# Kernel optimization log

Measured on AMD Instinct MI355X. Metric: run time of the kernel, lower is better.

The kernel has to match this reference:

```python
import jax, jax.numpy as jnp
import numpy as np

POOL = 7  # adaptive_avg_pool2d output size (7,7)


def _bin_edges(start, length):
    """Adaptive-avg-pool bin boundaries.
    start, length: [N] int32 -> (lo, hi) each [N, POOL] absolute indices,
    matching torch: lo_i = floor(i*L/P), hi_i = ceil((i+1)*L/P).
    """
    i = jnp.arange(POOL, dtype=jnp.int32)
    lo = start[:, None] + (i[None, :] * length[:, None]) // POOL
    hi = start[:, None] + (-((-(i[None, :] + 1)) * length[:, None] // POOL))
    # note: ceil(a/b) = -(-a // b); written below explicitly
    hi = start[:, None] - ((-(i[None, :] + 1) * length[:, None]) // POOL)
    return lo, hi


def roi_adaptive_avg_pool(features, rois):
    """features: [1, C, H, W]; rois: [N, 4] int (x1,y1,x2,y2 inclusive).
    Returns [N, C, POOL, POOL] == torch stack of adaptive_avg_pool2d over
    features[:, :, y1:y2+1, x1:x2+1], vectorized via an integral image.
    """
    B, C, H, W = features.shape  # B == 1 (forced by shared_fcs input dim)
    # integral image with a zero row/col prepended: ii[y, x] = sum over [:y, :x]
    ii = jnp.cumsum(jnp.cumsum(features, axis=2), axis=3)
    ii = jnp.pad(ii, ((0, 0), (0, 0), (1, 0), (1, 0)))[0]  # [C, H+1, W+1]

    x1, y1, x2, y2 = rois[:, 0], rois[:, 1], rois[:, 2], rois[:, 3]
    ys, ye = _bin_edges(y1, y2 - y1 + 1)   # [N, POOL]
    xs, xe = _bin_edges(x1, x2 - x1 + 1)
    Y0, Y1 = ys[:, :, None], ye[:, :, None]   # [N, POOL, 1]
    X0, X1 = xs[:, None, :], xe[:, None, :]   # [N, 1, POOL]

    def gather(Y, X):
        return ii[:, Y, X]  # [C, N, POOL, POOL]

    sums = gather(Y1, X1) - gather(Y0, X1) - gather(Y1, X0) + gather(Y0, X0)
    area = ((Y1 - Y0) * (X1 - X0)).astype(features.dtype)  # [N, POOL, POOL]
    pooled = sums / area[None]                              # [C, N, POOL, POOL]
    return jnp.transpose(pooled, (1, 0, 2, 3))              # [N, C, POOL, POOL]


def setup_inputs() -> dict:
    key = jax.random.key(0)
    ks = jax.random.split(key, 12)
    C, H, W, N, F = 256, 336, 336, 2000, 256
    features = jax.random.normal(ks[0], (1, C, H, W), dtype=jnp.float32)
    # valid small ROIs (shuttlecock-sized), x1<=x2, y1<=y2, in-bounds
    x1 = jax.random.randint(ks[1], (N,), 0, W - 40)
    y1 = jax.random.randint(ks[2], (N,), 0, H - 40)
    bw = jax.random.randint(ks[3], (N,), 4, 40)
    bh = jax.random.randint(ks[4], (N,), 4, 40)
    rois = jnp.stack([x1, y1, jnp.minimum(x1 + bw, W - 1),
                      jnp.minimum(y1 + bh, H - 1)], axis=1).astype(jnp.int32)
    d_in = C * POOL * POOL
    w1 = jax.random.normal(ks[5], (d_in, F), dtype=jnp.float32) * (1.0 / np.sqrt(d_in))
    b1 = jnp.zeros((F,), dtype=jnp.float32)
    w2 = jax.random.normal(ks[6], (F, F), dtype=jnp.float32) * (1.0 / np.sqrt(F))
    b2 = jnp.zeros((F,), dtype=jnp.float32)
    w_cls = jax.random.normal(ks[7], (F, 2), dtype=jnp.float32) * 0.01
    b_cls = jnp.zeros((2,), dtype=jnp.float32)
    w_reg = jax.random.normal(ks[8], (F, 4), dtype=jnp.float32) * 0.001
    b_reg = jnp.zeros((4,), dtype=jnp.float32)
    return {"features": features, "rois": rois, "w1": w1, "b1": b1,
            "w2": w2, "b2": b2, "w_cls": w_cls, "b_cls": b_cls,
            "w_reg": w_reg, "b_reg": b_reg}


def reference(features, rois, w1, b1, w2, b2, w_cls, b_cls, w_reg, b_reg):
    roi_feats = roi_adaptive_avg_pool(features, rois)          # [N, C, 7, 7]
    roi_feats = roi_feats.reshape(roi_feats.shape[0], -1)      # [N, C*49]
    h = jax.nn.relu(roi_feats @ w1 + b1)
    h = jax.nn.relu(h @ w2 + b2)
    cls_score = h @ w_cls + b_cls                              # [N, num_classes+1]
    bbox_pred = h @ w_reg + b_reg                              # [N, 4]
    return (cls_score, bbox_pred)
```

## Files before the change

kernel.cpp:

```cpp
#include <hip/hip_runtime.h>

typedef unsigned int uint;
typedef unsigned short ushort;
typedef __bf16 v8bf __attribute__((ext_vector_type(8)));
typedef float v4f __attribute__((ext_vector_type(4)));

#define CCH 256
#define HH 336
#define WW 336
#define HWSZ (HH*WW)
#define NROI 2000
#define KDIM 12544
#define MPAD 2048
#define SPLITK 14
#define KSP (KDIM/SPLITK)

__device__ __forceinline__ ushort bf16r(float f) {
  uint u = __float_as_uint(f);
  u += 0x7fffu + ((u >> 16) & 1u);
  return (ushort)(u >> 16);
}
__device__ __forceinline__ uint packbf(float a, float b) {
  return (uint)bf16r(a) | ((uint)bf16r(b) << 16);
}

typedef const __attribute__((address_space(1))) uint* gas_t;
typedef __attribute__((address_space(3))) uint* las_t;
__device__ __forceinline__ void async16(const void* g, void* l) {
  __builtin_amdgcn_global_load_lds((gas_t)g, (las_t)l, 16, 0, 0);
}

__global__ __launch_bounds__(256) void k_transpose(const float* __restrict__ f,
                                                   uint* __restrict__ ftu) {
  __shared__ uint T[64 * 132];
  int tid = threadIdx.x;
  int hw0 = blockIdx.x * 64;
  int hwl = tid & 63;
  int cq = tid >> 6;
  int hw = hw0 + hwl;
#pragma unroll 4
  for (int it = 0; it < 32; ++it) {
    int c = it * 8 + cq * 2;
    float a = f[(size_t)c * HWSZ + hw];
    float b = f[(size_t)(c + 1) * HWSZ + hw];
    T[hwl * 132 + it * 4 + cq] = packbf(a, b);
  }
  __syncthreads();
  int co = tid & 31, r = tid >> 5;
#pragma unroll
  for (int i = 0; i < 8; ++i) {
    int hwr = i * 8 + r;
    uint4 v = *(const uint4*)&T[hwr * 132 + co * 4];
    *(uint4*)(ftu + (size_t)(hw0 + hwr) * 128 + co * 4) = v;
  }
}

__global__ __launch_bounds__(256) void k_w1perm(const float* __restrict__ w1,
                                                uint* __restrict__ w1t_u) {
  int bin = blockIdx.x % 49;
  int c0 = (blockIdx.x / 49) * 32;
  __shared__ ushort T[32][258];
  int n = threadIdx.x;
  for (int i = 0; i < 32; ++i)
    T[i][n] = bf16r(w1[(size_t)((c0 + i) * 49 + bin) * 256 + n]);
  __syncthreads();
  int cc = threadIdx.x & 15;
  int nb = threadIdx.x >> 4;
  for (int rep = 0; rep < 16; ++rep) {
    int nn = rep * 16 + nb;
    uint v = (uint)T[2 * cc][nn] | ((uint)T[2 * cc + 1][nn] << 16);
    w1t_u[(size_t)nn * (KDIM / 2) + bin * 128 + c0 / 2 + cc] = v;
  }
}

__global__ __launch_bounds__(256) void k_w2t(const float* __restrict__ w2,
                                             ushort* __restrict__ w2t) {
  int n = blockIdx.x, k = threadIdx.x;
  w2t[n * 256 + k] = bf16r(w2[k * 256 + n]);
}

__global__ __launch_bounds__(256) void k_sort(const int* __restrict__ rois,
                                              int* __restrict__ perm) {
  __shared__ int hist[64];
  __shared__ int keys[NROI];
  int tid = threadIdx.x;
  if (tid < 64) hist[tid] = 0;
  __syncthreads();
  for (int i = tid; i < NROI; i += 256) {
    int x1 = rois[i * 4 + 0], y1 = rois[i * 4 + 1];
    int x2 = rois[i * 4 + 2], y2 = rois[i * 4 + 3];
    int cx = (x1 + x2) >> 1, cy = (y1 + y2) >> 1;
    int k = (cy / 42) * 8 + (cx / 42);
    keys[i] = k;
    atomicAdd(&hist[k], 1);
  }
  __syncthreads();
  if (tid == 0) {
    int s = 0;
    for (int b = 0; b < 64; ++b) { int c = hist[b]; hist[b] = s; s += c; }
  }
  __syncthreads();
  for (int i = tid; i < NROI; i += 256) {
    int pos = atomicAdd(&hist[keys[i]], 1);
    perm[pos] = i;
  }
}

#define UNPK8(u) do {                                        \
  a[0] += __uint_as_float((u).x << 16);                      \
  a[1] += __uint_as_float((u).x & 0xffff0000u);              \
  a[2] += __uint_as_float((u).y << 16);                      \
  a[3] += __uint_as_float((u).y & 0xffff0000u);              \
  a[4] += __uint_as_float((u).z << 16);                      \
  a[5] += __uint_as_float((u).z & 0xffff0000u);              \
  a[6] += __uint_as_float((u).w << 16);                      \
  a[7] += __uint_as_float((u).w & 0xffff0000u);              \
} while (0)

__global__ __launch_bounds__(448) void k_pool(const int* __restrict__ rois,
                                              const int* __restrict__ perm,
                                              const uint4* __restrict__ ft4,
                                              uint4* __restrict__ rf4) {
  int slot = (blockIdx.x & 7) * 250 + (blockIdx.x >> 3);
  int n = perm[slot];
  int wv = threadIdx.x >> 6;
  int t = threadIdx.x & 63;
  int co = t & 31, par = t >> 5;
  int x1 = rois[n * 4 + 0], y1 = rois[n * 4 + 1];
  int x2 = rois[n * 4 + 2], y2 = rois[n * 4 + 3];
  int Lw = x2 - x1 + 1, Lh = y2 - y1 + 1;
  int ylo = y1 + (wv * Lh) / 7;
  int yhi = y1 + ((wv + 1) * Lh + 6) / 7;
  int rh = yhi - ylo;
  uint ob = (uint)n * 1568 + (uint)wv * 224 + co;
  for (int b = 0; b < 7; ++b) {
    int lo = x1 + (b * Lw) / 7;
    int hi = x1 + ((b + 1) * Lw + 6) / 7;
    float a[8];
#pragma unroll
    for (int j = 0; j < 8; ++j) a[j] = 0.f;
    for (int y = ylo; y < yhi; ++y) {
      const uint4* p = ft4 + (size_t)(y * WW + lo + par) * 32 + co;
      for (int x = lo + par; x < hi; x += 2) {
        uint4 u = *p; p += 64;
        UNPK8(u);
      }
    }
#pragma unroll
    for (int j = 0; j < 8; ++j) a[j] += __shfl_xor(a[j], 32, 64);
    if (t < 32) {
      float inv = 1.0f / (float)(rh * (hi - lo));
      uint4 o;
      o.x = packbf(a[0] * inv, a[1] * inv);
      o.y = packbf(a[2] * inv, a[3] * inv);
      o.z = packbf(a[4] * inv, a[5] * inv);
      o.w = packbf(a[6] * inv, a[7] * inv);
      rf4[ob + b * 32] = o;
    }
  }
}

__global__ __launch_bounds__(256) void k_gemm1(const ushort* __restrict__ A,
                                               const ushort* __restrict__ B,
                                               float* __restrict__ P) {
  __shared__ ushort As[128 * 64];
  __shared__ ushort Bs[64 * 64];
  int m0 = blockIdx.x * 128;
  int n0 = blockIdx.y * 64;
  int ks = blockIdx.z;
  int k0 = ks * KSP;
  int tid = threadIdx.x;
  int lane = tid & 63, wv = tid >> 6;
  int wm = wv & 1, wn = wv >> 1;
  int lm = lane & 15, quad = lane >> 4;
  int srow = tid >> 3, scol = (tid & 7) * 8;
  v4f acc[4][2];
#pragma unroll
  for (int i = 0; i < 4; ++i)
#pragma unroll
    for (int j = 0; j < 2; ++j) acc[i][j] = (v4f){0.f, 0.f, 0.f, 0.f};
  const ushort* Ab = A + (size_t)(m0 + srow) * KDIM + k0 + scol;
  const ushort* Bb = B + (size_t)(n0 + srow) * KDIM + k0 + scol;
  for (int kt = 0; kt < KSP / 64; ++kt) {
    __syncthreads();
#pragma unroll
    for (int r = 0; r < 4; ++r)
      async16(Ab + (size_t)(r * 32) * KDIM + kt * 64, &As[(srow + r * 32) * 64 + scol]);
#pragma unroll
    for (int r = 0; r < 2; ++r)
      async16(Bb + (size_t)(r * 32) * KDIM + kt * 64, &Bs[(srow + r * 32) * 64 + scol]);
    __syncthreads();
#pragma unroll
    for (int kk = 0; kk < 64; kk += 32) {
      v8bf a[4], b[2];
#pragma unroll
      for (int i = 0; i < 4; ++i)
        a[i] = *(const v8bf*)&As[(wm * 64 + i * 16 + lm) * 64 + kk + quad * 8];
#pragma unroll
      for (int j = 0; j < 2; ++j)
        b[j] = *(const v8bf*)&Bs[(wn * 32 + j * 16 + lm) * 64 + kk + quad * 8];
#pragma unroll
      for (int i = 0; i < 4; ++i)
#pragma unroll
        for (int j = 0; j < 2; ++j)
          acc[i][j] = __builtin_amdgcn_mfma_f32_16x16x32_bf16(a[i], b[j], acc[i][j], 0, 0, 0);
    }
  }
  float* Pb = P + (size_t)ks * MPAD * 256;
#pragma unroll
  for (int i = 0; i < 4; ++i)
#pragma unroll
    for (int j = 0; j < 2; ++j) {
      int row = m0 + wm * 64 + i * 16 + quad * 4;
      int col = n0 + wn * 32 + j * 16 + lm;
#pragma unroll
      for (int r = 0; r < 4; ++r)
        Pb[(size_t)(row + r) * 256 + col] = acc[i][j][r];
    }
}

__global__ __launch_bounds__(256) void k_reduce(const float* __restrict__ P,
                                                const float* __restrict__ b1,
                                                uint* __restrict__ h1u) {
  int idx = blockIdx.x * 256 + threadIdx.x;
  int m = idx >> 7, np = idx & 127;
  const float2* Pp = (const float2*)P;
  float2 s = {0.f, 0.f};
#pragma unroll
  for (int ks = 0; ks < SPLITK; ++ks) {
    float2 v = Pp[(size_t)(ks * MPAD + m) * 128 + np];
    s.x += v.x; s.y += v.y;
  }
  s.x += b1[2 * np]; s.y += b1[2 * np + 1];
  s.x = fmaxf(s.x, 0.f); s.y = fmaxf(s.y, 0.f);
  h1u[idx] = packbf(s.x, s.y);
}

__global__ __launch_bounds__(256) void k_gemm2(const ushort* __restrict__ h1b,
                                               const ushort* __restrict__ w2t,
                                               const float* __restrict__ b2,
                                               const float* __restrict__ wcls,
                                               const float* __restrict__ bcls,
                                               const float* __restrict__ wreg,
                                               const float* __restrict__ breg,
                                               float* __restrict__ out) {
  __shared__ ushort As2[64 * 64];
  __shared__ ushort Bs2[256 * 64];
  __shared__ float Hs[64 * 257];
  int tid = threadIdx.x;
  int r0 = blockIdx.x * 64;
  int lane = tid & 63, wv = tid >> 6;
  int lm = lane & 15, quad = lane >> 4;
  int srow = tid >> 3, scol = (tid & 7) * 8;
  v4f acc[16];
#pragma unroll
  for (int j = 0; j < 16; ++j) acc[j] = (v4f){0.f, 0.f, 0.f, 0.f};
  for (int kt = 0; kt < 4; ++kt) {
    __syncthreads();
#pragma unroll
    for (int r = 0; r < 2; ++r)
      async16(h1b + (size_t)(r0 + srow + r * 32) * 256 + kt * 64 + scol,
              &As2[(srow + r * 32) * 64 + scol]);
#pragma unroll
    for (int r = 0; r < 8; ++r)
      async16(w2t + (size_t)(srow + r * 32) * 256 + kt * 64 + scol,
              &Bs2[(srow + r * 32) * 64 + scol]);
    __syncthreads();
#pragma unroll
    for (int kk = 0; kk < 64; kk += 32) {
      v8bf a = *(const v8bf*)&As2[(wv * 16 + lm) * 64 + kk + quad * 8];
#pragma unroll
      for (int j = 0; j < 16; ++j) {
        v8bf b = *(const v8bf*)&Bs2[(j * 16 + lm) * 64 + kk + quad * 8];
        acc[j] = __builtin_amdgcn_mfma_f32_16x16x32_bf16(a, b, acc[j], 0, 0, 0);
      }
    }
  }
#pragma unroll
  for (int j = 0; j < 16; ++j) {
    int nn = j * 16 + lm;
    float bb = b2[nn];
#pragma unroll
    for (int r = 0; r < 4; ++r) {
      int row = wv * 16 + quad * 4 + r;
      Hs[row * 257 + nn] = fmaxf(acc[j][r] + bb, 0.f);
    }
  }
  __syncthreads();
  for (int o = tid; o < 384; o += 256) {
    int hd = o >> 6, r = o & 63;
    int grow = r0 + r;
    float d = 0.f;
    if (hd < 2) {
      for (int k = 0; k < 256; ++k) d += Hs[r * 257 + k] * wcls[k * 2 + hd];
      d += bcls[hd];
      if (grow < NROI) out[grow * 2 + hd] = d;
    } else {
      int h4 = hd - 2;
      for (int k = 0; k < 256; ++k) d += Hs[r * 257 + k] * wreg[k * 4 + h4];
      d += breg[h4];
      if (grow < NROI) out[4000 + grow * 4 + h4] = d;
    }
  }
}

extern "C" void kernel_launch(void* const* d_in, const int* in_sizes, int n_in,
                              void* d_out, int out_size, void* d_ws, size_t ws_size,
                              hipStream_t stream) {
  const float* features = (const float*)d_in[0];
  const int* rois = (const int*)d_in[1];
  const float* w1 = (const float*)d_in[2];
  const float* b1 = (const float*)d_in[3];
  const float* w2 = (const float*)d_in[4];
  const float* b2 = (const float*)d_in[5];
  const float* wcls = (const float*)d_in[6];
  const float* bcls = (const float*)d_in[7];
  const float* wreg = (const float*)d_in[8];
  const float* breg = (const float*)d_in[9];
  char* ws = (char*)d_ws;
  ushort* ft  = (ushort*)(ws + 0);
  ushort* w1t = (ushort*)(ws + 57802752);
  ushort* w2t = (ushort*)(ws + 64225280);
  ushort* rf  = (ushort*)(ws + 64356352);
  int*    perm = (int*)(ws + 64356352 + (size_t)NROI * KDIM * 2);
  float*  P   = (float*)(ws + 115736576);
  ushort* h1b = (ushort*)(ws + 145096704);
  float* out = (float*)d_out;

  hipLaunchKernelGGL(k_transpose, dim3(HWSZ / 64), dim3(256), 0, stream,
                     features, (uint*)ft);
  hipLaunchKernelGGL(k_w1perm, dim3(392), dim3(256), 0, stream, w1, (uint*)w1t);
  hipLaunchKernelGGL(k_w2t, dim3(256), dim3(256), 0, stream, w2, w2t);
  hipLaunchKernelGGL(k_sort, dim3(1), dim3(256), 0, stream, rois, perm);
  hipLaunchKernelGGL(k_pool, dim3(NROI), dim3(448), 0, stream, rois, perm,
                     (const uint4*)ft, (uint4*)rf);
  hipLaunchKernelGGL(k_gemm1, dim3(16, 4, SPLITK), dim3(256), 0, stream, rf, w1t, P);
  hipLaunchKernelGGL(k_reduce, dim3(1024), dim3(256), 0, stream, P, b1, (uint*)h1b);
  hipLaunchKernelGGL(k_gemm2, dim3(32), dim3(256), 0, stream, h1b, w2t, b2, wcls, bcls, wreg, breg, out);
}
```

Baseline: 370.4 us.

## Split pool blocks per row-bin, unroll pooling loads, widen gemm1 N tile

```diff
diff --git a/kernel.cpp b/kernel.cpp
--- a/kernel.cpp
+++ b/kernel.cpp
@@ -106,25 +106,26 @@
   }
 }
 
-#define UNPK8(u) do {                                        \
-  a[0] += __uint_as_float((u).x << 16);                      \
-  a[1] += __uint_as_float((u).x & 0xffff0000u);              \
-  a[2] += __uint_as_float((u).y << 16);                      \
-  a[3] += __uint_as_float((u).y & 0xffff0000u);              \
-  a[4] += __uint_as_float((u).z << 16);                      \
-  a[5] += __uint_as_float((u).z & 0xffff0000u);              \
-  a[6] += __uint_as_float((u).w << 16);                      \
-  a[7] += __uint_as_float((u).w & 0xffff0000u);              \
+#define UNPK8(A, u) do {                                     \
+  A[0] += __uint_as_float((u).x << 16);                      \
+  A[1] += __uint_as_float((u).x & 0xffff0000u);              \
+  A[2] += __uint_as_float((u).y << 16);                      \
+  A[3] += __uint_as_float((u).y & 0xffff0000u);              \
+  A[4] += __uint_as_float((u).z << 16);                      \
+  A[5] += __uint_as_float((u).z & 0xffff0000u);              \
+  A[6] += __uint_as_float((u).w << 16);                      \
+  A[7] += __uint_as_float((u).w & 0xffff0000u);              \
 } while (0)
 
-__global__ __launch_bounds__(448) void k_pool(const int* __restrict__ rois,
-                                              const int* __restrict__ perm,
-                                              const uint4* __restrict__ ft4,
-                                              uint4* __restrict__ rf4) {
-  int slot = (blockIdx.x & 7) * 250 + (blockIdx.x >> 3);
+__global__ __launch_bounds__(64) void k_pool(const int* __restrict__ rois,
+                                             const int* __restrict__ perm,
+                                             const uint4* __restrict__ ft4,
+                                             uint4* __restrict__ rf4) {
+  int bx = blockIdx.x;
+  int slot = (bx & 7) * 250 + (bx >> 3);
   int n = perm[slot];
-  int wv = threadIdx.x >> 6;
-  int t = threadIdx.x & 63;
+  int wv = blockIdx.y;
+  int t = threadIdx.x;
   int co = t & 31, par = t >> 5;
   int x1 = rois[n * 4 + 0], y1 = rois[n * 4 + 1];
   int x2 = rois[n * 4 + 2], y2 = rois[n * 4 + 3];
@@ -136,16 +137,26 @@
   for (int b = 0; b < 7; ++b) {
     int lo = x1 + (b * Lw) / 7;
     int hi = x1 + ((b + 1) * Lw + 6) / 7;
-    float a[8];
-#pragma unroll
-    for (int j = 0; j < 8; ++j) a[j] = 0.f;
+    float a[8], c[8];
+#pragma unroll
+    for (int j = 0; j < 8; ++j) { a[j] = 0.f; c[j] = 0.f; }
     for (int y = ylo; y < yhi; ++y) {
       const uint4* p = ft4 + (size_t)(y * WW + lo + par) * 32 + co;
-      for (int x = lo + par; x < hi; x += 2) {
-        uint4 u = *p; p += 64;
-        UNPK8(u);
+      int x = lo + par;
+      for (; x + 2 < hi; x += 4) {
+        uint4 u0 = p[0], u1 = p[64];
+        p += 128;
+        UNPK8(a, u0);
+        UNPK8(c, u1);
       }
-    }
+      for (; x < hi; x += 2) {
+        uint4 u = p[0];
+        p += 64;
+        UNPK8(a, u);
+      }
+    }
+#pragma unroll
+    for (int j = 0; j < 8; ++j) a[j] += c[j];
 #pragma unroll
     for (int j = 0; j < 8; ++j) a[j] += __shfl_xor(a[j], 32, 64);
     if (t < 32) {
@@ -164,21 +175,21 @@
                                                const ushort* __restrict__ B,
                                                float* __restrict__ P) {
   __shared__ ushort As[128 * 64];
-  __shared__ ushort Bs[64 * 64];
+  __shared__ ushort Bs[128 * 64];
   int m0 = blockIdx.x * 128;
-  int n0 = blockIdx.y * 64;
+  int n0 = blockIdx.y * 128;
   int ks = blockIdx.z;
   int k0 = ks * KSP;
   int tid = threadIdx.x;
   int lane = tid & 63, wv = tid >> 6;
-  int wm = wv & 1, wn = wv >> 1;
+  int wm = wv >> 1, wn = wv & 1;
   int lm = lane & 15, quad = lane >> 4;
   int srow = tid >> 3, scol = (tid & 7) * 8;
-  v4f acc[4][2];
+  v4f acc[4][4];
 #pragma unroll
   for (int i = 0; i < 4; ++i)
 #pragma unroll
-    for (int j = 0; j < 2; ++j) acc[i][j] = (v4f){0.f, 0.f, 0.f, 0.f};
+    for (int j = 0; j < 4; ++j) acc[i][j] = (v4f){0.f, 0.f, 0.f, 0.f};
   const ushort* Ab = A + (size_t)(m0 + srow) * KDIM + k0 + scol;
   const ushort* Bb = B + (size_t)(n0 + srow) * KDIM + k0 + scol;
   for (int kt = 0; kt < KSP / 64; ++kt) {
@@ -187,22 +198,22 @@
     for (int r = 0; r < 4; ++r)
       async16(Ab + (size_t)(r * 32) * KDIM + kt * 64, &As[(srow + r * 32) * 64 + scol]);
 #pragma unroll
-    for (int r = 0; r < 2; ++r)
+    for (int r = 0; r < 4; ++r)
       async16(Bb + (size_t)(r * 32) * KDIM + kt * 64, &Bs[(srow + r * 32) * 64 + scol]);
     __syncthreads();
 #pragma unroll
     for (int kk = 0; kk < 64; kk += 32) {
-      v8bf a[4], b[2];
+      v8bf a[4], b[4];
 #pragma unroll
       for (int i = 0; i < 4; ++i)
         a[i] = *(const v8bf*)&As[(wm * 64 + i * 16 + lm) * 64 + kk + quad * 8];
 #pragma unroll
-      for (int j = 0; j < 2; ++j)
-        b[j] = *(const v8bf*)&Bs[(wn * 32 + j * 16 + lm) * 64 + kk + quad * 8];
+      for (int j = 0; j < 4; ++j)
+        b[j] = *(const v8bf*)&Bs[(wn * 64 + j * 16 + lm) * 64 + kk + quad * 8];
 #pragma unroll
       for (int i = 0; i < 4; ++i)
 #pragma unroll
-        for (int j = 0; j < 2; ++j)
+        for (int j = 0; j < 4; ++j)
           acc[i][j] = __builtin_amdgcn_mfma_f32_16x16x32_bf16(a[i], b[j], acc[i][j], 0, 0, 0);
     }
   }
@@ -210,9 +221,9 @@
 #pragma unroll
   for (int i = 0; i < 4; ++i)
 #pragma unroll
-    for (int j = 0; j < 2; ++j) {
+    for (int j = 0; j < 4; ++j) {
       int row = m0 + wm * 64 + i * 16 + quad * 4;
-      int col = n0 + wn * 32 + j * 16 + lm;
+      int col = n0 + wn * 64 + j * 16 + lm;
 #pragma unroll
       for (int r = 0; r < 4; ++r)
         Pb[(size_t)(row + r) * 256 + col] = acc[i][j][r];
@@ -332,9 +343,9 @@
   hipLaunchKernelGGL(k_w1perm, dim3(392), dim3(256), 0, stream, w1, (uint*)w1t);
   hipLaunchKernelGGL(k_w2t, dim3(256), dim3(256), 0, stream, w2, w2t);
   hipLaunchKernelGGL(k_sort, dim3(1), dim3(256), 0, stream, rois, perm);
-  hipLaunchKernelGGL(k_pool, dim3(NROI), dim3(448), 0, stream, rois, perm,
+  hipLaunchKernelGGL(k_pool, dim3(NROI, 7), dim3(64), 0, stream, rois, perm,
                      (const uint4*)ft, (uint4*)rf);
-  hipLaunchKernelGGL(k_gemm1, dim3(16, 4, SPLITK), dim3(256), 0, stream, rf, w1t, P);
+  hipLaunchKernelGGL(k_gemm1, dim3(16, 2, SPLITK), dim3(256), 0, stream, rf, w1t, P);
   hipLaunchKernelGGL(k_reduce, dim3(1024), dim3(256), 0, stream, P, b1, (uint*)h1b);
   hipLaunchKernelGGL(k_gemm2, dim3(32), dim3(256), 0, stream, h1b, w2t, b2, wcls, bcls, wreg, breg, out);
 }
```

New measurement: 354.0 us. 4.4% less time.
